# Kernel optimization log

Measured on AMD Instinct MI355X. Metric: run time of the kernel, lower is better.

The kernel has to match this reference:

```python
import jax, jax.numpy as jnp
import numpy as np

B, T, F, D = 8, 2048, 512, 256

def setup_inputs() -> dict:
    key = jax.random.key(0)
    k1, k2, k3, k4 = jax.random.split(key, 4)
    scale = 1.0 / np.sqrt(F)
    return {
        "inputs": jax.random.normal(k1, (B, T, F), dtype=jnp.float32),
        "W_q": jax.random.normal(k2, (F, D), dtype=jnp.float32) * scale,
        "W_k": jax.random.normal(k3, (F, D), dtype=jnp.float32) * scale,
        "W_v": jax.random.normal(k4, (F, D), dtype=jnp.float32) * scale,
    }

def reference(inputs, W_q, W_k, W_v):
    # Q,K,V: [B,T,D]
    Q = jnp.einsum('btf,fd->btd', inputs, W_q)
    K = jnp.einsum('btf,fd->btd', inputs, W_k)
    V = jnp.einsum('btf,fd->btd', inputs, W_v)
    d = Q.shape[-1]
    scores = jnp.einsum('bqd,bkd->bqk', Q, K) / jnp.sqrt(jnp.asarray(d, dtype=Q.dtype))
    attn = jax.nn.softmax(scores, axis=-1)  # [B,T,T]
    return jnp.einsum('bqk,bkd->bqd', attn, V)
```

## Files before the change

kernel.cpp:

```cpp
#include <hip/hip_runtime.h>
#include <cstdint>
#include <cstddef>

#define B_ 8
#define T_ 2048
#define F_ 512
#define D_ 256
#define NSPLIT 2
#define KVB 32
#define NT ((T_ / NSPLIT) / KVB)

typedef float f32x4 __attribute__((ext_vector_type(4)));
typedef __bf16 bf16x8 __attribute__((ext_vector_type(8)));
typedef unsigned short us8 __attribute__((ext_vector_type(8)));
typedef unsigned short us4 __attribute__((ext_vector_type(4)));

static __device__ __forceinline__ unsigned short f2bf(float f) {
  union { float f; unsigned int u; } v; v.f = f;
  unsigned int u = v.u;
  u += 0x7fffu + ((u >> 16) & 1u);
  return (unsigned short)(u >> 16);
}

static __device__ __forceinline__ float bf2f(unsigned short s) {
  union { float f; unsigned int u; } v; v.u = ((unsigned int)s) << 16;
  return v.f;
}

static __device__ __forceinline__ bf16x8 ldb8(const unsigned short* p) {
  return *reinterpret_cast<const bf16x8*>(p);
}

static __device__ __forceinline__ f32x4 mfma_bf16(bf16x8 a, bf16x8 b, f32x4 c) {
  return __builtin_amdgcn_mfma_f32_16x16x32_bf16(a, b, c, 0, 0, 0);
}

static __device__ __forceinline__ void gload_lds16(const unsigned short* g,
                                                   unsigned short* l) {
  __builtin_amdgcn_global_load_lds(
      (const __attribute__((address_space(1))) void*)g,
      (__attribute__((address_space(3))) void*)l, 16, 0, 0);
}

__global__ __launch_bounds__(256) void xb_kernel(const float* __restrict__ X,
                                                 unsigned short* __restrict__ Xb) {
  size_t i = ((size_t)blockIdx.x * 256 + threadIdx.x) * 8;
  float4 a = *reinterpret_cast<const float4*>(&X[i]);
  float4 b = *reinterpret_cast<const float4*>(&X[i + 4]);
  us8 p;
  p[0] = f2bf(a.x); p[1] = f2bf(a.y); p[2] = f2bf(a.z); p[3] = f2bf(a.w);
  p[4] = f2bf(b.x); p[5] = f2bf(b.y); p[6] = f2bf(b.z); p[7] = f2bf(b.w);
  *reinterpret_cast<us8*>(&Xb[i]) = p;
}

__global__ __launch_bounds__(256) void tw_kernel(const float* __restrict__ Wq,
                                                 const float* __restrict__ Wk,
                                                 const float* __restrict__ Wv,
                                                 unsigned short* __restrict__ Wt) {
  __shared__ unsigned short tile[64][72];
  const float* W = (blockIdx.z == 0) ? Wq : (blockIdx.z == 1) ? Wk : Wv;
  unsigned short* out = Wt + (size_t)blockIdx.z * (D_ * F_);
  int k0 = blockIdx.x * 64, n0 = blockIdx.y * 64;
  int t = threadIdx.x;
#pragma unroll
  for (int i = 0; i < 4; i++) {
    int c = t + 256 * i;
    int r = c >> 4, c4 = (c & 15) * 4;
    float4 v = *reinterpret_cast<const float4*>(&W[(size_t)(k0 + r) * D_ + n0 + c4]);
    us4 p; p[0] = f2bf(v.x); p[1] = f2bf(v.y); p[2] = f2bf(v.z); p[3] = f2bf(v.w);
    *reinterpret_cast<us4*>(&tile[r][c4]) = p;
  }
  __syncthreads();
#pragma unroll
  for (int i = 0; i < 4; i++) {
    int c = t + 256 * i;
    int r = c >> 4, c4 = (c & 15) * 4;
    us4 p;
    p[0] = tile[c4 + 0][r];
    p[1] = tile[c4 + 1][r];
    p[2] = tile[c4 + 2][r];
    p[3] = tile[c4 + 3][r];
    *reinterpret_cast<us4*>(&out[(size_t)(n0 + r) * F_ + k0 + c4]) = p;
  }
}

__global__ __launch_bounds__(256) void proj_kernel(const unsigned short* __restrict__ Xb,
                                                   const unsigned short* __restrict__ Wt,
                                                   unsigned short* __restrict__ Qs,
                                                   unsigned short* __restrict__ Kb,
                                                   unsigned short* __restrict__ Vt) {
  __shared__ unsigned short Au[2][128 * 64];
  __shared__ unsigned short Bu[2][128 * 64];
  const int brow = blockIdx.x * 128;
  const int bcol = blockIdx.y * 128;
  const int z = blockIdx.z;
  const unsigned short* W = Wt + (size_t)z * (D_ * F_);
  const int tid = threadIdx.x;
  const int wave = tid >> 6, lane = tid & 63;
  const int wr = wave >> 1, wc = wave & 1;
  const int lg = lane >> 4, lr = lane & 15;

  f32x4 acc[4][4] = {};

  auto stageT = [&](unsigned short* dst, const unsigned short* srcBase, int k0) {
#pragma unroll
    for (int i = 0; i < 4; i++) {
      int L = (tid + 256 * i) * 16;
      int r = L >> 7;
      int c = L & 127;
      int csw = c ^ ((r & 7) << 4);
      gload_lds16(srcBase + (size_t)r * F_ + k0 + (csw >> 1), dst + (L >> 1));
    }
  };

  stageT(Au[0], Xb + (size_t)brow * F_, 0);
  stageT(Bu[0], W + (size_t)bcol * F_, 0);
  __syncthreads();

  for (int ks = 0; ks < 8; ks++) {
    const int cur = ks & 1;
    if (ks + 1 < 8) {
      stageT(Au[cur ^ 1], Xb + (size_t)brow * F_, (ks + 1) * 64);
      stageT(Bu[cur ^ 1], W + (size_t)bcol * F_, (ks + 1) * 64);
    }
#pragma unroll
    for (int kk = 0; kk < 2; kk++) {
      bf16x8 af[4], bfr[4];
#pragma unroll
      for (int mi = 0; mi < 4; mi++) {
        int r = wr * 64 + mi * 16 + lr;
        af[mi] = ldb8(&Au[cur][r * 64 + ((((kk * 64 + lg * 16) ^ ((r & 7) << 4))) >> 1)]);
      }
#pragma unroll
      for (int ni = 0; ni < 4; ni++) {
        int r = wc * 64 + ni * 16 + lr;
        bfr[ni] = ldb8(&Bu[cur][r * 64 + ((((kk * 64 + lg * 16) ^ ((r & 7) << 4))) >> 1)]);
      }
#pragma unroll
      for (int mi = 0; mi < 4; mi++)
#pragma unroll
        for (int ni = 0; ni < 4; ni++)
          acc[mi][ni] = mfma_bf16(af[mi], bfr[ni], acc[mi][ni]);
    }
    __syncthreads();
  }

#pragma unroll
  for (int mi = 0; mi < 4; mi++) {
#pragma unroll
    for (int ni = 0; ni < 4; ni++) {
      int row0 = brow + wr * 64 + mi * 16 + lg * 4;
      int col = bcol + wc * 64 + ni * 16 + lr;
      if (z == 0) {
#pragma unroll
        for (int j = 0; j < 4; j++)
          Qs[(size_t)(row0 + j) * D_ + col] = f2bf(acc[mi][ni][j] * 0.0625f);
      } else if (z == 1) {
#pragma unroll
        for (int j = 0; j < 4; j++)
          Kb[(size_t)(row0 + j) * D_ + col] = f2bf(acc[mi][ni][j]);
      } else {
        int b = row0 >> 11, t0 = row0 & (T_ - 1);
        us4 p;
#pragma unroll
        for (int j = 0; j < 4; j++) p[j] = f2bf(acc[mi][ni][j]);
        *reinterpret_cast<us4*>(&Vt[(size_t)b * D_ * T_ + (size_t)col * T_ + t0]) = p;
      }
    }
  }
}

__global__ __launch_bounds__(256)
void flash_kernel(const unsigned short* __restrict__ Qs,
                  const unsigned short* __restrict__ Kb,
                  const unsigned short* __restrict__ Vt,
                  unsigned short* __restrict__ op,
                  float2* __restrict__ ml) {
  __shared__ unsigned short Kl[2][KVB * 256];
  __shared__ unsigned short Vl[2][256 * KVB];
  __shared__ unsigned short Pl[4][16][40];

  const int b = blockIdx.x, qt = blockIdx.y, h = blockIdx.z;
  const int tid = threadIdx.x;
  const int wave = tid >> 6, lane = tid & 63;
  const int lg = lane >> 4, lr = lane & 15;

  const int qrow = qt * 64 + wave * 16 + lr;
  const unsigned short* qptr = Qs + ((size_t)b * T_ + qrow) * D_;
  bf16x8 qf[8];
#pragma unroll
  for (int ks = 0; ks < 8; ks++) qf[ks] = ldb8(qptr + ks * 32 + lg * 8);

  f32x4 o[16] = {};
  float m = -__builtin_inff();
  float lsum = 0.f;

  const int keyoff = h * (T_ / NSPLIT);
  const unsigned short* kbase = Kb + (size_t)b * T_ * D_ + (size_t)keyoff * D_;
  const unsigned short* vbase = Vt + (size_t)b * D_ * T_;

  auto stage = [&](int buf, int kt) {
    const unsigned short* ksrc = kbase + (size_t)kt * KVB * D_;
#pragma unroll
    for (int i = 0; i < 4; i++) {
      int L = (tid + 256 * i) * 16;
      int r = L >> 9;
      int c = L & 511;
      int csw = c ^ ((r & 7) << 4);
      gload_lds16(ksrc + r * 256 + (csw >> 1), &Kl[buf][L >> 1]);
    }
    const int key0 = keyoff + kt * KVB;
#pragma unroll
    for (int i = 0; i < 4; i++) {
      int L = (tid + 256 * i) * 16;
      int d = L >> 6;
      int c = L & 63;
      int csw = c ^ (((d >> 1) & 3) << 4);
      gload_lds16(vbase + (size_t)d * T_ + key0 + (csw >> 1), &Vl[buf][L >> 1]);
    }
  };

  stage(0, 0);
  __syncthreads();

  for (int kt = 0; kt < NT; kt++) {
    const int cur = kt & 1;
    if (kt + 1 < NT) stage(cur ^ 1, kt + 1);

    f32x4 s[2] = {};
    __builtin_amdgcn_s_setprio(1);
#pragma unroll
    for (int ks = 0; ks < 8; ks++) {
#pragma unroll
      for (int nf = 0; nf < 2; nf++) {
        int r = nf * 16 + lr;
        bf16x8 kb = ldb8(&Kl[cur][r * 256 + (((ks * 64 + lg * 16) ^ ((r & 7) << 4)) >> 1)]);
        s[nf] = mfma_bf16(kb, qf[ks], s[nf]);
      }
    }
    __builtin_amdgcn_s_setprio(0);

    float pm;
    {
      float a0 = fmaxf(fmaxf(s[0][0], s[0][1]), fmaxf(s[0][2], s[0][3]));
      float a1 = fmaxf(fmaxf(s[1][0], s[1][1]), fmaxf(s[1][2], s[1][3]));
      pm = fmaxf(a0, a1);
      pm = fmaxf(pm, __shfl_xor(pm, 16));
      pm = fmaxf(pm, __shfl_xor(pm, 32));
    }
    if (!__all(pm - m <= 8.0f)) {
      float mn = fmaxf(m, pm);
      float corr = __expf(m - mn);
      m = mn;
      lsum *= corr;
      float c4[4];
#pragma unroll
      for (int j = 0; j < 4; j++) c4[j] = __shfl(corr, lg * 4 + j);
#pragma unroll
      for (int nf = 0; nf < 16; nf++)
#pragma unroll
        for (int j = 0; j < 4; j++) o[nf][j] *= c4[j];
    }
    float rs = 0.f;
#pragma unroll
    for (int nf = 0; nf < 2; nf++) {
      us4 pk;
#pragma unroll
      for (int j = 0; j < 4; j++) {
        float p = __expf(s[nf][j] - m);
        rs += p;
        pk[j] = f2bf(p);
      }
      *reinterpret_cast<us4*>(&Pl[wave][lr][nf * 16 + lg * 4]) = pk;
    }
    rs += __shfl_xor(rs, 16);
    rs += __shfl_xor(rs, 32);
    lsum += rs;

    __builtin_amdgcn_s_setprio(1);
    {
      bf16x8 pa = ldb8(&Pl[wave][lr][lg * 8]);
#pragma unroll
      for (int nf = 0; nf < 16; nf++) {
        int d = nf * 16 + lr;
        bf16x8 vb = ldb8(&Vl[cur][d * 32 + (((lg * 16) ^ (((d >> 1) & 3) << 4)) >> 1)]);
        o[nf] = mfma_bf16(pa, vb, o[nf]);
      }
    }
    __builtin_amdgcn_s_setprio(0);

    __syncthreads();
  }

  const size_t rowbase = (size_t)h * (B_ * T_) + (size_t)b * T_;
#pragma unroll
  for (int nf = 0; nf < 16; nf++) {
#pragma unroll
    for (int j = 0; j < 4; j++) {
      int q = qt * 64 + wave * 16 + lg * 4 + j;
      op[(rowbase + q) * D_ + nf * 16 + lr] = f2bf(o[nf][j]);
    }
  }
  if (lg == 0) {
    int q = qt * 64 + wave * 16 + lr;
    ml[rowbase + q] = make_float2(m, lsum);
  }
}

__global__ __launch_bounds__(256) void merge_kernel(const unsigned short* __restrict__ op,
                                                    const float2* __restrict__ ml,
                                                    float* __restrict__ out) {
  const int tid = threadIdx.x;
  const int row = blockIdx.x * 4 + (tid >> 6);
  const int d0 = (tid & 63) * 4;

  float mh[NSPLIT], lh[NSPLIT];
  float M = -__builtin_inff();
#pragma unroll
  for (int hh = 0; hh < NSPLIT; hh++) {
    float2 v = ml[(size_t)hh * (B_ * T_) + row];
    mh[hh] = v.x; lh[hh] = v.y;
    M = fmaxf(M, v.x);
  }
  float e[NSPLIT], den = 0.f;
#pragma unroll
  for (int hh = 0; hh < NSPLIT; hh++) {
    e[hh] = __expf(mh[hh] - M);
    den += e[hh] * lh[hh];
  }
  const float inv = 1.0f / den;

  float acc[4] = {0.f, 0.f, 0.f, 0.f};
#pragma unroll
  for (int hh = 0; hh < NSPLIT; hh++) {
    us4 p = *reinterpret_cast<const us4*>(
        &op[((size_t)hh * (B_ * T_) + row) * D_ + d0]);
#pragma unroll
    for (int j = 0; j < 4; j++) acc[j] += e[hh] * bf2f(p[j]);
  }
  float4 r;
  r.x = acc[0] * inv; r.y = acc[1] * inv; r.z = acc[2] * inv; r.w = acc[3] * inv;
  *reinterpret_cast<float4*>(&out[(size_t)row * D_ + d0]) = r;
}

extern "C" void kernel_launch(void* const* d_in, const int* in_sizes, int n_in,
                              void* d_out, int out_size, void* d_ws, size_t ws_size,
                              hipStream_t stream) {
  const float* X  = (const float*)d_in[0];
  const float* Wq = (const float*)d_in[1];
  const float* Wk = (const float*)d_in[2];
  const float* Wv = (const float*)d_in[3];
  float* out = (float*)d_out;

  char* ws = (char*)d_ws;
  unsigned short* Wt = (unsigned short*)ws;
  unsigned short* Qs = (unsigned short*)(ws + 786432);
  unsigned short* Kb = (unsigned short*)(ws + 786432 + 8388608);
  unsigned short* Vt = (unsigned short*)(ws + 786432 + 2 * 8388608);
  unsigned short* op = (unsigned short*)(ws + 786432 + 3 * 8388608);
  unsigned short* Xb = op;
  float2* ml        = (float2*)(ws + 786432 + 3 * 8388608 + (size_t)NSPLIT * B_ * T_ * D_ * 2);

  xb_kernel<<<dim3((B_ * T_ * F_) / (256 * 8)), 256, 0, stream>>>(X, Xb);
  tw_kernel<<<dim3(F_ / 64, D_ / 64, 3), 256, 0, stream>>>(Wq, Wk, Wv, Wt);
  proj_kernel<<<dim3((B_ * T_) / 128, D_ / 128, 3), 256, 0, stream>>>(Xb, Wt, Qs, Kb, Vt);
  flash_kernel<<<dim3(B_, T_ / 64, NSPLIT), 256, 0, stream>>>(Qs, Kb, Vt, op, ml);
  merge_kernel<<<dim3(B_ * T_ / 4), 256, 0, stream>>>(op, ml, out);
}
```

Before: 106.6 us.

## Process two query row groups per wave and double the key split count

Each wave now owns 32 query rows as two 16-row groups. Every K and V fragment read from LDS feeds two MFMAs, which halves LDS and global K/V traffic per unit of work. The query tile per block grows from 64 to 128 rows, and NSPLIT goes from 2 to 4 so the grid keeps the same number of blocks. The cost is twice the accumulator and query registers, which may lower occupancy, plus a larger partial-output buffer and more work in the merge kernel.

```diff
diff --git a/kernel.cpp b/kernel.cpp
--- a/kernel.cpp
+++ b/kernel.cpp
@@ -6,7 +6,7 @@
 #define T_ 2048
 #define F_ 512
 #define D_ 256
-#define NSPLIT 2
+#define NSPLIT 4
 #define KVB 32
 #define NT ((T_ / NSPLIT) / KVB)
 
@@ -178,22 +178,26 @@
                   float2* __restrict__ ml) {
   __shared__ unsigned short Kl[2][KVB * 256];
   __shared__ unsigned short Vl[2][256 * KVB];
-  __shared__ unsigned short Pl[4][16][40];
+  __shared__ unsigned short Pl[4][2][16][36];
 
   const int b = blockIdx.x, qt = blockIdx.y, h = blockIdx.z;
   const int tid = threadIdx.x;
   const int wave = tid >> 6, lane = tid & 63;
   const int lg = lane >> 4, lr = lane & 15;
 
-  const int qrow = qt * 64 + wave * 16 + lr;
-  const unsigned short* qptr = Qs + ((size_t)b * T_ + qrow) * D_;
-  bf16x8 qf[8];
-#pragma unroll
-  for (int ks = 0; ks < 8; ks++) qf[ks] = ldb8(qptr + ks * 32 + lg * 8);
-
-  f32x4 o[16] = {};
-  float m = -__builtin_inff();
-  float lsum = 0.f;
+  const int qbase = qt * 128 + wave * 32;
+  const unsigned short* qp0 = Qs + ((size_t)b * T_ + qbase + lr) * D_;
+  const unsigned short* qp1 = Qs + ((size_t)b * T_ + qbase + 16 + lr) * D_;
+  bf16x8 qf0[8], qf1[8];
+#pragma unroll
+  for (int ks = 0; ks < 8; ks++) {
+    qf0[ks] = ldb8(qp0 + ks * 32 + lg * 8);
+    qf1[ks] = ldb8(qp1 + ks * 32 + lg * 8);
+  }
+
+  f32x4 o0[16] = {}, o1[16] = {};
+  float m0 = -__builtin_inff(), m1 = -__builtin_inff();
+  float l0 = 0.f, l1 = 0.f;
 
   const int keyoff = h * (T_ / NSPLIT);
   const unsigned short* kbase = Kb + (size_t)b * T_ * D_ + (size_t)keyoff * D_;
@@ -220,26 +224,7 @@
     }
   };
 
-  stage(0, 0);
-  __syncthreads();
-
-  for (int kt = 0; kt < NT; kt++) {
-    const int cur = kt & 1;
-    if (kt + 1 < NT) stage(cur ^ 1, kt + 1);
-
-    f32x4 s[2] = {};
-    __builtin_amdgcn_s_setprio(1);
-#pragma unroll
-    for (int ks = 0; ks < 8; ks++) {
-#pragma unroll
-      for (int nf = 0; nf < 2; nf++) {
-        int r = nf * 16 + lr;
-        bf16x8 kb = ldb8(&Kl[cur][r * 256 + (((ks * 64 + lg * 16) ^ ((r & 7) << 4)) >> 1)]);
-        s[nf] = mfma_bf16(kb, qf[ks], s[nf]);
-      }
-    }
-    __builtin_amdgcn_s_setprio(0);
-
+  auto softmax = [&](f32x4 (&s)[2], float& m, float& lsum, f32x4 (&o)[16], int g) {
     float pm;
     {
       float a0 = fmaxf(fmaxf(s[0][0], s[0][1]), fmaxf(s[0][2], s[0][3]));
@@ -271,24 +256,49 @@
         rs += p;
         pk[j] = f2bf(p);
       }
-      *reinterpret_cast<us4*>(&Pl[wave][lr][nf * 16 + lg * 4]) = pk;
+      *reinterpret_cast<us4*>(&Pl[wave][g][lr][nf * 16 + lg * 4]) = pk;
     }
     rs += __shfl_xor(rs, 16);
     rs += __shfl_xor(rs, 32);
     lsum += rs;
-
+  };
+
+  stage(0, 0);
+  __syncthreads();
+
+  for (int kt = 0; kt < NT; kt++) {
+    const int cur = kt & 1;
+    if (kt + 1 < NT) stage(cur ^ 1, kt + 1);
+
+    f32x4 s0[2] = {}, s1[2] = {};
     __builtin_amdgcn_s_setprio(1);
-    {
-      bf16x8 pa = ldb8(&Pl[wave][lr][lg * 8]);
-#pragma unroll
-      for (int nf = 0; nf < 16; nf++) {
-        int d = nf * 16 + lr;
-        bf16x8 vb = ldb8(&Vl[cur][d * 32 + (((lg * 16) ^ (((d >> 1) & 3) << 4)) >> 1)]);
-        o[nf] = mfma_bf16(pa, vb, o[nf]);
+#pragma unroll
+    for (int ks = 0; ks < 8; ks++) {
+#pragma unroll
+      for (int nf = 0; nf < 2; nf++) {
+        int r = nf * 16 + lr;
+        bf16x8 kb = ldb8(&Kl[cur][r * 256 + (((ks * 64 + lg * 16) ^ ((r & 7) << 4)) >> 1)]);
+        s0[nf] = mfma_bf16(kb, qf0[ks], s0[nf]);
+        s1[nf] = mfma_bf16(kb, qf1[ks], s1[nf]);
       }
     }
     __builtin_amdgcn_s_setprio(0);
 
+    softmax(s0, m0, l0, o0, 0);
+    softmax(s1, m1, l1, o1, 1);
+
+    bf16x8 pa0 = ldb8(&Pl[wave][0][lr][lg * 8]);
+    bf16x8 pa1 = ldb8(&Pl[wave][1][lr][lg * 8]);
+    __builtin_amdgcn_s_setprio(1);
+#pragma unroll
+    for (int nf = 0; nf < 16; nf++) {
+      int d = nf * 16 + lr;
+      bf16x8 vb = ldb8(&Vl[cur][d * 32 + (((lg * 16) ^ (((d >> 1) & 3) << 4)) >> 1)]);
+      o0[nf] = mfma_bf16(pa0, vb, o0[nf]);
+      o1[nf] = mfma_bf16(pa1, vb, o1[nf]);
+    }
+    __builtin_amdgcn_s_setprio(0);
+
     __syncthreads();
   }
 
@@ -297,13 +307,14 @@
   for (int nf = 0; nf < 16; nf++) {
 #pragma unroll
     for (int j = 0; j < 4; j++) {
-      int q = qt * 64 + wave * 16 + lg * 4 + j;
-      op[(rowbase + q) * D_ + nf * 16 + lr] = f2bf(o[nf][j]);
+      int q0 = qbase + lg * 4 + j;
+      op[(rowbase + q0) * D_ + nf * 16 + lr] = f2bf(o0[nf][j]);
+      op[(rowbase + q0 + 16) * D_ + nf * 16 + lr] = f2bf(o1[nf][j]);
     }
   }
   if (lg == 0) {
-    int q = qt * 64 + wave * 16 + lr;
-    ml[rowbase + q] = make_float2(m, lsum);
+    ml[rowbase + qbase + lr] = make_float2(m0, l0);
+    ml[rowbase + qbase + 16 + lr] = make_float2(m1, l1);
   }
 }
 
@@ -364,6 +375,6 @@
   xb_kernel<<<dim3((B_ * T_ * F_) / (256 * 8)), 256, 0, stream>>>(X, Xb);
   tw_kernel<<<dim3(F_ / 64, D_ / 64, 3), 256, 0, stream>>>(Wq, Wk, Wv, Wt);
   proj_kernel<<<dim3((B_ * T_) / 128, D_ / 128, 3), 256, 0, stream>>>(Xb, Wt, Qs, Kb, Vt);
-  flash_kernel<<<dim3(B_, T_ / 64, NSPLIT), 256, 0, stream>>>(Qs, Kb, Vt, op, ml);
+  flash_kernel<<<dim3(B_, T_ / 128, NSPLIT), 256, 0, stream>>>(Qs, Kb, Vt, op, ml);
   merge_kernel<<<dim3(B_ * T_ / 4), 256, 0, stream>>>(op, ml, out);
 }
```

Result: slower. 132.1 us (+23.9%).
